# Optimization experiments

Measured on AMD Instinct MI355X. Metric: run time of the kernel, lower is better.

Reference implementation:

```python
import jax, jax.numpy as jnp
import numpy as np

B, N, C = 128, 8732, 21  # batch, SSD priors, VOC classes (incl. background)
EPS = 1e-7


def setup_inputs() -> dict:
    key = jax.random.key(0)
    k1, k2, k3 = jax.random.split(key, 3)
    return {
        "lam": jnp.float32(0.7),
        "conf": jax.random.uniform(k1, (B, N, C), dtype=jnp.float32),
        "conf_shuffle": jax.random.uniform(k2, (B, N, C), dtype=jnp.float32),
        "conf_interpolation": jax.random.uniform(k3, (B, N, C), dtype=jnp.float32),
    }


def reference(lam, conf, conf_shuffle, conf_interpolation):
    half = conf.shape[0] // 2
    # swap the two halves of the shuffled batch
    conf_temp = jnp.concatenate([conf_shuffle[half:], conf_shuffle[:half]], axis=0)

    # foreground mask: max class score beats background score, on both sides
    left_mask = jnp.max(conf[..., 1:], axis=-1) > conf[..., 0]
    right_mask = jnp.max(conf_temp[..., 1:], axis=-1) > conf_temp[..., 0]
    mask = (left_mask & right_mask).astype(conf.dtype)  # [B, N]

    mixed = lam * conf + (1.0 - lam) * conf_temp + EPS
    inter = conf_interpolation + EPS

    sg = jax.lax.stop_gradient
    # KLDivLoss(log_input, target) = target * (log(target) - log_input), summed over classes
    inter_t = sg(inter)
    kl_a = jnp.sum(inter_t * (jnp.log(inter_t) - jnp.log(mixed)), axis=-1)  # [B, N]
    mixed_t = sg(mixed)
    kl_b = jnp.sum(mixed_t * (jnp.log(mixed_t) - jnp.log(inter)), axis=-1)  # [B, N]

    cnt = jnp.sum(mask)
    # masked mean over selected (b, n) samples; 0 if mask empty
    loss = jnp.sum((kl_a + kl_b) * mask) / jnp.maximum(cnt, 1.0)
    return jnp.where(cnt > 0, loss / 2.0, jnp.float32(0.0))
```

## Files before the change

### kernel.cpp

```cpp
#include <hip/hip_runtime.h>


#define EPS 1e-7f

constexpr int B = 128;
constexpr int N = 8732;
constexpr int C = 21;
constexpr int ROWS = B * N;
constexpr int GRID = 1024;
constexpr int BLOCK = 256;

__global__ __launch_bounds__(BLOCK) void isd_main_kernel(
    const float* __restrict__ lam_p,
    const float* __restrict__ conf,
    const float* __restrict__ csh,
    const float* __restrict__ cin,
    double* __restrict__ partials)
{
    const float lam = lam_p[0];
    const float oml = 1.0f - lam;

    float sum = 0.0f;
    float cnt = 0.0f;

    const int stride = gridDim.x * blockDim.x;
    for (int r = blockIdx.x * blockDim.x + threadIdx.x; r < ROWS; r += stride) {
        const int b  = r / N;
        const int n  = r - b * N;
        const int b2 = b ^ (B / 2);

        const float* pc = conf + (size_t)r * C;
        const float* pt = csh  + ((size_t)b2 * N + n) * C;
        const float* pi = cin  + (size_t)r * C;

        float c0 = 0.0f, t0 = 0.0f;
        float cmax = -1e30f, tmax = -1e30f;
        float kl = 0.0f;

        #pragma unroll
        for (int c = 0; c < C; ++c) {
            const float cv = pc[c];
            const float tv = pt[c];
            const float iv = pi[c] + EPS;
            const float mv = fmaf(lam, cv, oml * tv) + EPS;
            const float lm = __logf(mv);
            const float li = __logf(iv);
            kl += (iv - mv) * (li - lm);
            if (c == 0) { c0 = cv; t0 = tv; }
            else        { cmax = fmaxf(cmax, cv); tmax = fmaxf(tmax, tv); }
        }

        const float msk = ((cmax > c0) && (tmax > t0)) ? 1.0f : 0.0f;
        sum += kl * msk;
        cnt += msk;
    }

    #pragma unroll
    for (int off = 32; off > 0; off >>= 1) {
        sum += __shfl_down(sum, off, 64);
        cnt += __shfl_down(cnt, off, 64);
    }

    __shared__ float s_sum[BLOCK / 64];
    __shared__ float s_cnt[BLOCK / 64];
    const int wave = threadIdx.x >> 6;
    const int lane = threadIdx.x & 63;
    if (lane == 0) { s_sum[wave] = sum; s_cnt[wave] = cnt; }
    __syncthreads();

    if (threadIdx.x == 0) {
        double bs = 0.0, bc = 0.0;
        #pragma unroll
        for (int w = 0; w < BLOCK / 64; ++w) { bs += (double)s_sum[w]; bc += (double)s_cnt[w]; }
        partials[2 * blockIdx.x + 0] = bs;
        partials[2 * blockIdx.x + 1] = bc;
    }
}

__global__ __launch_bounds__(64) void isd_final_kernel(
    const double* __restrict__ partials,
    float* __restrict__ out)
{
    double s = 0.0, c = 0.0;
    for (int i = threadIdx.x; i < GRID; i += 64) {
        s += partials[2 * i + 0];
        c += partials[2 * i + 1];
    }
    #pragma unroll
    for (int off = 32; off > 0; off >>= 1) {
        s += __shfl_down(s, off, 64);
        c += __shfl_down(c, off, 64);
    }
    if (threadIdx.x == 0) {
        float loss = 0.0f;
        if (c > 0.0) loss = (float)(s / fmax(c, 1.0) * 0.5);
        out[0] = loss;
    }
}

extern "C" void kernel_launch(void* const* d_in, const int* in_sizes, int n_in,
                              void* d_out, int out_size, void* d_ws, size_t ws_size,
                              hipStream_t stream) {
    const float* lam  = (const float*)d_in[0];
    const float* conf = (const float*)d_in[1];
    const float* csh  = (const float*)d_in[2];
    const float* cin  = (const float*)d_in[3];
    float* out = (float*)d_out;
    double* partials = (double*)d_ws;

    isd_main_kernel<<<GRID, BLOCK, 0, stream>>>(lam, conf, csh, cin, partials);
    isd_final_kernel<<<1, 64, 0, stream>>>(partials, out);
}
```

Before: 278.2 us.

## Stage row tiles through LDS with coalesced float4 loads

Result: no change. 274.7 us (-1.3%).

```diff
diff --git a/kernel.cpp b/kernel.cpp
--- a/kernel.cpp
+++ b/kernel.cpp
@@ -7,8 +7,12 @@
 constexpr int N = 8732;
 constexpr int C = 21;
 constexpr int ROWS = B * N;
-constexpr int GRID = 1024;
+constexpr int TILE = 256;
 constexpr int BLOCK = 256;
+constexpr int GRID = ROWS / TILE;
+constexpr int TILE_ELEMS = TILE * C;
+constexpr int TILE_F4 = TILE_ELEMS / 4;
+constexpr int BATCH_F4 = (N * C) / 4;
 
 __global__ __launch_bounds__(BLOCK) void isd_main_kernel(
     const float* __restrict__ lam_p,
@@ -17,43 +21,52 @@
     const float* __restrict__ cin,
     double* __restrict__ partials)
 {
+    __shared__ float s_conf[TILE_ELEMS];
+    __shared__ float s_csh [TILE_ELEMS];
+    __shared__ float s_cin [TILE_ELEMS];
+
+    const int tid = threadIdx.x;
+    const int tileF4base = blockIdx.x * TILE_F4;
+
+    const float4* conf4 = (const float4*)conf;
+    const float4* csh4  = (const float4*)csh;
+    const float4* cin4  = (const float4*)cin;
+
+    for (int k = tid; k < TILE_F4; k += BLOCK) {
+        const int G = tileF4base + k;
+        ((float4*)s_conf)[k] = conf4[G];
+        ((float4*)s_cin )[k] = cin4[G];
+        const int b  = G / BATCH_F4;
+        const int G2 = G + ((b ^ 64) - b) * BATCH_F4;
+        ((float4*)s_csh)[k] = csh4[G2];
+    }
+    __syncthreads();
+
     const float lam = lam_p[0];
     const float oml = 1.0f - lam;
 
-    float sum = 0.0f;
-    float cnt = 0.0f;
+    const float* pc = s_conf + tid * C;
+    const float* pt = s_csh  + tid * C;
+    const float* pi = s_cin  + tid * C;
 
-    const int stride = gridDim.x * blockDim.x;
-    for (int r = blockIdx.x * blockDim.x + threadIdx.x; r < ROWS; r += stride) {
-        const int b  = r / N;
-        const int n  = r - b * N;
-        const int b2 = b ^ (B / 2);
+    float c0 = 0.0f, t0 = 0.0f;
+    float cmax = -1e30f, tmax = -1e30f;
+    float kl = 0.0f;
 
-        const float* pc = conf + (size_t)r * C;
-        const float* pt = csh  + ((size_t)b2 * N + n) * C;
-        const float* pi = cin  + (size_t)r * C;
+    #pragma unroll
+    for (int c = 0; c < C; ++c) {
+        const float cv = pc[c];
+        const float tv = pt[c];
+        const float iv = pi[c] + EPS;
+        const float mv = fmaf(lam, cv, oml * tv) + EPS;
+        kl += (iv - mv) * (__logf(iv) - __logf(mv));
+        if (c == 0) { c0 = cv; t0 = tv; }
+        else        { cmax = fmaxf(cmax, cv); tmax = fmaxf(tmax, tv); }
+    }
 
-        float c0 = 0.0f, t0 = 0.0f;
-        float cmax = -1e30f, tmax = -1e30f;
-        float kl = 0.0f;
-
-        #pragma unroll
-        for (int c = 0; c < C; ++c) {
-            const float cv = pc[c];
-            const float tv = pt[c];
-            const float iv = pi[c] + EPS;
-            const float mv = fmaf(lam, cv, oml * tv) + EPS;
-            const float lm = __logf(mv);
-            const float li = __logf(iv);
-            kl += (iv - mv) * (li - lm);
-            if (c == 0) { c0 = cv; t0 = tv; }
-            else        { cmax = fmaxf(cmax, cv); tmax = fmaxf(tmax, tv); }
-        }
-
-        const float msk = ((cmax > c0) && (tmax > t0)) ? 1.0f : 0.0f;
-        sum += kl * msk;
-        cnt += msk;
-    }
+    const float msk = ((cmax > c0) && (tmax > t0)) ? 1.0f : 0.0f;
+    float sum = kl * msk;
+    float cnt = msk;
 
     #pragma unroll
     for (int off = 32; off > 0; off >>= 1) {
@@ -61,28 +74,28 @@
         cnt += __shfl_down(cnt, off, 64);
     }
 
-    __shared__ float s_sum[BLOCK / 64];
-    __shared__ float s_cnt[BLOCK / 64];
-    const int wave = threadIdx.x >> 6;
-    const int lane = threadIdx.x & 63;
-    if (lane == 0) { s_sum[wave] = sum; s_cnt[wave] = cnt; }
+    __shared__ float r_sum[BLOCK / 64];
+    __shared__ float r_cnt[BLOCK / 64];
+    const int wave = tid >> 6;
+    const int lane = tid & 63;
+    if (lane == 0) { r_sum[wave] = sum; r_cnt[wave] = cnt; }
     __syncthreads();
 
-    if (threadIdx.x == 0) {
+    if (tid == 0) {
         double bs = 0.0, bc = 0.0;
         #pragma unroll
-        for (int w = 0; w < BLOCK / 64; ++w) { bs += (double)s_sum[w]; bc += (double)s_cnt[w]; }
+        for (int w = 0; w < BLOCK / 64; ++w) { bs += (double)r_sum[w]; bc += (double)r_cnt[w]; }
         partials[2 * blockIdx.x + 0] = bs;
         partials[2 * blockIdx.x + 1] = bc;
     }
 }
 
-__global__ __launch_bounds__(64) void isd_final_kernel(
+__global__ __launch_bounds__(256) void isd_final_kernel(
     const double* __restrict__ partials,
     float* __restrict__ out)
 {
     double s = 0.0, c = 0.0;
-    for (int i = threadIdx.x; i < GRID; i += 64) {
+    for (int i = threadIdx.x; i < GRID; i += 256) {
         s += partials[2 * i + 0];
         c += partials[2 * i + 1];
     }
@@ -91,10 +104,15 @@
         s += __shfl_down(s, off, 64);
         c += __shfl_down(c, off, 64);
     }
+    __shared__ double ss[4], sc[4];
+    const int wave = threadIdx.x >> 6;
+    const int lane = threadIdx.x & 63;
+    if (lane == 0) { ss[wave] = s; sc[wave] = c; }
+    __syncthreads();
     if (threadIdx.x == 0) {
-        float loss = 0.0f;
-        if (c > 0.0) loss = (float)(s / fmax(c, 1.0) * 0.5);
-        out[0] = loss;
+        const double S  = ss[0] + ss[1] + ss[2] + ss[3];
+        const double Cc = sc[0] + sc[1] + sc[2] + sc[3];
+        out[0] = (Cc > 0.0) ? (float)(S / fmax(Cc, 1.0) * 0.5) : 0.0f;
     }
 }
 
@@ -109,5 +127,5 @@
     double* partials = (double*)d_ws;
 
     isd_main_kernel<<<GRID, BLOCK, 0, stream>>>(lam, conf, csh, cin, partials);
-    isd_final_kernel<<<1, 64, 0, stream>>>(partials, out);
+    isd_final_kernel<<<1, 256, 0, stream>>>(partials, out);
 }
```

## Coalesce row loads via per-wave LDS staging of 64-row chunks

Applied to the files above, without the earlier changes.

Result: no change. 283.5 us (+1.9%).

```diff
diff --git a/kernel.cpp b/kernel.cpp
--- a/kernel.cpp
+++ b/kernel.cpp
@@ -7,31 +7,54 @@
 constexpr int N = 8732;
 constexpr int C = 21;
 constexpr int ROWS = B * N;
-constexpr int GRID = 1024;
-constexpr int BLOCK = 256;
+constexpr int CHUNK_ROWS = 64;
+constexpr int CHUNK_ELEMS = CHUNK_ROWS * C;
+constexpr int CHUNKS_PER_WAVE = 8;
+constexpr int GRID = ROWS / (CHUNK_ROWS * CHUNKS_PER_WAVE);
+constexpr int HALF_ELEMS = (B / 2) * N * C;
 
-__global__ __launch_bounds__(BLOCK) void isd_main_kernel(
+__global__ __launch_bounds__(64) void isd_main_kernel(
     const float* __restrict__ lam_p,
     const float* __restrict__ conf,
     const float* __restrict__ csh,
     const float* __restrict__ cin,
     double* __restrict__ partials)
 {
+    __shared__ float s_conf[CHUNK_ELEMS];
+    __shared__ float s_csh [CHUNK_ELEMS];
+    __shared__ float s_cin [CHUNK_ELEMS];
+
+    const int lane = threadIdx.x;
     const float lam = lam_p[0];
     const float oml = 1.0f - lam;
 
     float sum = 0.0f;
     float cnt = 0.0f;
 
-    const int stride = gridDim.x * blockDim.x;
-    for (int r = blockIdx.x * blockDim.x + threadIdx.x; r < ROWS; r += stride) {
-        const int b  = r / N;
-        const int n  = r - b * N;
-        const int b2 = b ^ (B / 2);
+    const int chunk0 = blockIdx.x * CHUNKS_PER_WAVE;
 
-        const float* pc = conf + (size_t)r * C;
-        const float* pt = csh  + ((size_t)b2 * N + n) * C;
-        const float* pi = cin  + (size_t)r * C;
+    for (int ci = 0; ci < CHUNKS_PER_WAVE; ++ci) {
+        const int base = (chunk0 + ci) * CHUNK_ELEMS;
+
+        float rc[C], rs[C], ri[C];
+        #pragma unroll
+        for (int k = 0; k < C; ++k) {
+            const int e = base + k * 64 + lane;
+            rc[k] = conf[e];
+            ri[k] = cin[e];
+            const int e2 = (e < HALF_ELEMS) ? (e + HALF_ELEMS) : (e - HALF_ELEMS);
+            rs[k] = csh[e2];
+        }
+        #pragma unroll
+        for (int k = 0; k < C; ++k) {
+            s_conf[k * 64 + lane] = rc[k];
+            s_csh [k * 64 + lane] = rs[k];
+            s_cin [k * 64 + lane] = ri[k];
+        }
+
+        const float* pc = s_conf + lane * C;
+        const float* pt = s_csh  + lane * C;
+        const float* pi = s_cin  + lane * C;
 
         float c0 = 0.0f, t0 = 0.0f;
         float cmax = -1e30f, tmax = -1e30f;
@@ -43,9 +66,7 @@
             const float tv = pt[c];
             const float iv = pi[c] + EPS;
             const float mv = fmaf(lam, cv, oml * tv) + EPS;
-            const float lm = __logf(mv);
-            const float li = __logf(iv);
-            kl += (iv - mv) * (li - lm);
+            kl += (iv - mv) * (__logf(iv) - __logf(mv));
             if (c == 0) { c0 = cv; t0 = tv; }
             else        { cmax = fmaxf(cmax, cv); tmax = fmaxf(tmax, tv); }
         }
@@ -61,28 +82,18 @@
         cnt += __shfl_down(cnt, off, 64);
     }
 
-    __shared__ float s_sum[BLOCK / 64];
-    __shared__ float s_cnt[BLOCK / 64];
-    const int wave = threadIdx.x >> 6;
-    const int lane = threadIdx.x & 63;
-    if (lane == 0) { s_sum[wave] = sum; s_cnt[wave] = cnt; }
-    __syncthreads();
-
-    if (threadIdx.x == 0) {
-        double bs = 0.0, bc = 0.0;
-        #pragma unroll
-        for (int w = 0; w < BLOCK / 64; ++w) { bs += (double)s_sum[w]; bc += (double)s_cnt[w]; }
-        partials[2 * blockIdx.x + 0] = bs;
-        partials[2 * blockIdx.x + 1] = bc;
+    if (lane == 0) {
+        partials[2 * blockIdx.x + 0] = (double)sum;
+        partials[2 * blockIdx.x + 1] = (double)cnt;
     }
 }
 
-__global__ __launch_bounds__(64) void isd_final_kernel(
+__global__ __launch_bounds__(256) void isd_final_kernel(
     const double* __restrict__ partials,
     float* __restrict__ out)
 {
     double s = 0.0, c = 0.0;
-    for (int i = threadIdx.x; i < GRID; i += 64) {
+    for (int i = threadIdx.x; i < GRID; i += 256) {
         s += partials[2 * i + 0];
         c += partials[2 * i + 1];
     }
@@ -91,10 +102,15 @@
         s += __shfl_down(s, off, 64);
         c += __shfl_down(c, off, 64);
     }
+    __shared__ double ss[4], sc[4];
+    const int wave = threadIdx.x >> 6;
+    const int lane = threadIdx.x & 63;
+    if (lane == 0) { ss[wave] = s; sc[wave] = c; }
+    __syncthreads();
     if (threadIdx.x == 0) {
-        float loss = 0.0f;
-        if (c > 0.0) loss = (float)(s / fmax(c, 1.0) * 0.5);
-        out[0] = loss;
+        const double S  = ss[0] + ss[1] + ss[2] + ss[3];
+        const double Cc = sc[0] + sc[1] + sc[2] + sc[3];
+        out[0] = (Cc > 0.0) ? (float)(S / fmax(Cc, 1.0) * 0.5) : 0.0f;
     }
 }
 
@@ -108,6 +124,6 @@
     float* out = (float*)d_out;
     double* partials = (double*)d_ws;
 
-    isd_main_kernel<<<GRID, BLOCK, 0, stream>>>(lam, conf, csh, cin, partials);
-    isd_final_kernel<<<1, 64, 0, stream>>>(partials, out);
+    isd_main_kernel<<<GRID, 64, 0, stream>>>(lam, conf, csh, cin, partials);
+    isd_final_kernel<<<1, 256, 0, stream>>>(partials, out);
 }
```
